# Optimization experiments

Measured on AMD Instinct MI355X. Metric: run time of the kernel, lower is better.

Reference implementation:

```python
import jax, jax.numpy as jnp
import numpy as np

D_MODEL = 192
D_INNER = 384          # expand(2) * d_model
HEADDIM = 12
NHEADS = 32            # d_inner // headdim
DSTATE = 16
NGROUPS = 1
CONV_DIM = D_INNER + 2 * NGROUPS * DSTATE          # 416
D_IN_PROJ = 2 * D_INNER + 2 * NGROUPS * DSTATE + NHEADS  # 832
LN_EPS = 1e-5


def silu(x):
    return x * jax.nn.sigmoid(x)


def depthwise_conv2d(x_nchw, w, b):
    # groups == channels depthwise conv, kernel 3, padding 1 (SAME)
    out = jax.lax.conv_general_dilated(
        x_nchw, w, window_strides=(1, 1), padding='SAME',
        feature_group_count=CONV_DIM,
        dimension_numbers=('NCHW', 'OIHW', 'NCHW'))
    return out + b[None, :, None, None]


def setup_inputs() -> dict:
    key = jax.random.key(0)
    ks = jax.random.split(key, 10)
    Bn, H, W = 4, 128, 128
    u = jax.random.normal(ks[0], (Bn, H, W, D_MODEL), jnp.float32)
    t = jax.random.normal(ks[1], (Bn, H, W, D_MODEL), jnp.float32)
    s_in = 1.0 / np.sqrt(D_MODEL)
    W_in = jax.random.normal(ks[2], (D_IN_PROJ, D_MODEL), jnp.float32) * s_in
    W_t_in = jax.random.normal(ks[3], (D_IN_PROJ, D_MODEL), jnp.float32) * s_in
    conv_w = jax.random.normal(ks[4], (CONV_DIM, 1, 3, 3), jnp.float32) * (1.0 / 3.0)
    conv_b = jnp.zeros((CONV_DIM,), jnp.float32)
    # dt_bias = inverse-softplus of dt sampled log-uniform in [dt_min, dt_max]
    dt0 = jnp.exp(jax.random.uniform(ks[5], (NHEADS,)) * (np.log(0.1) - np.log(0.001)) + np.log(0.001))
    dt_bias = dt0 + jnp.log(-jnp.expm1(-dt0))
    A_log = jnp.log(jax.random.uniform(ks[6], (NHEADS,), minval=1.0, maxval=16.0))
    D = jnp.ones((NHEADS,), jnp.float32)
    ln_gamma = jnp.ones((D_INNER,), jnp.float32)
    ln_beta = jnp.zeros((D_INNER,), jnp.float32)
    W_out = jax.random.normal(ks[7], (D_MODEL, D_INNER), jnp.float32) * (1.0 / np.sqrt(D_INNER))
    return dict(u=u, t=t, W_in=W_in, W_t_in=W_t_in, conv_w=conv_w, conv_b=conv_b,
                dt_bias=dt_bias, A_log=A_log, D=D, ln_gamma=ln_gamma, ln_beta=ln_beta,
                W_out=W_out)


def reference(u, t, W_in, W_t_in, conv_w, conv_b, dt_bias, A_log, D,
              ln_gamma, ln_beta, W_out):
    B0, H, W_, C0 = u.shape
    L = H * W_
    uu = u.reshape(B0, L, C0)
    tt = t.reshape(B0, L, C0)

    # in_proj on main branch: split into z, xBC, dt
    zxbcdt = uu @ W_in.T                                    # (B, L, 832)
    z = zxbcdt[..., :D_INNER]                               # (B, L, 384)
    xBC = zxbcdt[..., D_INNER:D_INNER + CONV_DIM]           # (B, L, 416)
    dt = zxbcdt[..., D_INNER + CONV_DIM:]                   # (B, L, 32)
    dt = jax.nn.softplus(dt + dt_bias)

    # t branch: only x1B1C1 part is ultimately used (C := C1)
    x1B1C1 = (tt @ W_t_in.T)[..., D_INNER:D_INNER + CONV_DIM]

    # depthwise 3x3 conv + silu on both branches
    xBC = xBC.reshape(B0, H, W_, CONV_DIM).transpose(0, 3, 1, 2)
    xBC = silu(depthwise_conv2d(xBC, conv_w, conv_b))
    xBC = xBC.transpose(0, 2, 3, 1).reshape(B0, L, CONV_DIM)

    x1B1C1 = x1B1C1.reshape(B0, H, W_, CONV_DIM).transpose(0, 3, 1, 2)
    x1B1C1 = silu(depthwise_conv2d(x1B1C1, conv_w, conv_b))
    x1B1C1 = x1B1C1.transpose(0, 2, 3, 1).reshape(B0, L, CONV_DIM)

    x = xBC[..., :D_INNER]                                  # V features (B, L, 384)
    Bk = xBC[..., D_INNER:D_INNER + NGROUPS * DSTATE]       # K (B, L, 16)
    Cq = x1B1C1[..., D_INNER + NGROUPS * DSTATE:]           # Q from t-branch (B, L, 16)

    A = -jnp.exp(A_log)                                     # (nheads,), negative

    # non-causal linear attention duality (ngroups == 1)
    V = x.reshape(B0, L, NHEADS, HEADDIM).transpose(0, 2, 1, 3)   # (B, h, L, d)
    dtT = dt.transpose(0, 2, 1)                                   # (B, h, L)
    dA = -(dtT[..., None] * A[None, :, None, None])               # ssd_positve_dA: positive
    V_scaled = V * dA
    KV = jnp.einsum('bln,bhld->bhnd', Bk, V_scaled)               # (B, h, 16, 12)
    y = jnp.einsum('bln,bhnd->bhld', Cq, KV) + V * D[None, :, None, None]
    y = y.transpose(0, 2, 1, 3).reshape(B0, L, D_INNER)

    # LayerNorm over d_inner
    mu = jnp.mean(y, axis=-1, keepdims=True)
    var = jnp.mean((y - mu) ** 2, axis=-1, keepdims=True)
    y = (y - mu) * jax.lax.rsqrt(var + LN_EPS) * ln_gamma + ln_beta

    y = y * z
    out = y @ W_out.T
    return out.reshape(B0, H, W_, C0)
```

## Files before the change

kernel.cpp:

```cpp
#include <hip/hip_runtime.h>
#include <hip/hip_bf16.h>
#include <math.h>


#define BN 4
#define HH 128
#define WWID 128
#define LTOK (HH*WWID)
#define NTOK (BN*LTOK)
#define DMODEL 192
#define DINNER 384
#define NH 32
#define HD 12
#define DST 16
#define CONVD 416
#define KVCHUNKS 64
#define PM 256
#define PBN 64
#define BSTR 200

typedef __hip_bfloat16 bf16;
typedef unsigned int uint32;
typedef unsigned short ushort16;
typedef __attribute__((ext_vector_type(8))) short bf16x8;
typedef __attribute__((ext_vector_type(4))) float f32x4;
typedef __attribute__((ext_vector_type(16))) float f32x16;

__device__ __forceinline__ float bflo(uint32 v){ return __uint_as_float((v & 0xffffu) << 16); }
__device__ __forceinline__ float bfhi(uint32 v){ return __uint_as_float(v & 0xffff0000u); }
__device__ __forceinline__ ushort16 f2bf(float f){
    __hip_bfloat16 h = __float2bfloat16(f);
    return *reinterpret_cast<const ushort16*>(&h);
}
__device__ __forceinline__ float softplusf(float x){
    return (x > 20.f) ? x : log1pf(expf(x));
}
__device__ __forceinline__ float siluf(float x){
    return x / (1.f + expf(-x));
}

union BFPK { short s[8]; bf16x8 v; };

__global__ __launch_bounds__(256) void k_prep(
    const float* __restrict__ Win, const float* __restrict__ Wout,
    const float* __restrict__ cw,
    bf16* __restrict__ Winbf, bf16* __restrict__ Woutbf, float* __restrict__ wtr)
{
    const int i = blockIdx.x*256 + threadIdx.x;
    if (i < 832*DMODEL)   Winbf[i]  = __float2bfloat16(Win[i]);
    if (i < DMODEL*DINNER) Woutbf[i] = __float2bfloat16(Wout[i]);
    if (i < CONVD*9) { const int c = i/9, k = i - c*9; wtr[k*420 + c] = cw[i]; }
}

__global__ __launch_bounds__(512) void k_proj_mfma(
    const float* __restrict__ u, const bf16* __restrict__ Wbf,
    const float* __restrict__ dt_b, const float* __restrict__ A_log,
    bf16* __restrict__ z_bf, bf16* __restrict__ xbc_pre, float* __restrict__ dA)
{
    __shared__ __align__(16) short S[2][PBN*BSTR];

    const int tid = threadIdx.x;
    const int m0 = blockIdx.x * PM;
    const int wid = tid >> 6, lane = tid & 63;
    const int fr = lane & 31;
    const int hi = lane >> 5;

    bf16x8 a[12];
    {
        const float* arow = u + (size_t)(m0 + wid*32 + fr)*DMODEL;
        #pragma unroll
        for (int ks=0;ks<12;++ks) {
            const float4 a0 = *(const float4*)(arow + ks*16 + hi*8);
            const float4 a1 = *(const float4*)(arow + ks*16 + hi*8 + 4);
            BFPK pk;
            pk.s[0]=(short)f2bf(a0.x); pk.s[1]=(short)f2bf(a0.y);
            pk.s[2]=(short)f2bf(a0.z); pk.s[3]=(short)f2bf(a0.w);
            pk.s[4]=(short)f2bf(a1.x); pk.s[5]=(short)f2bf(a1.y);
            pk.s[6]=(short)f2bf(a1.z); pk.s[7]=(short)f2bf(a1.w);
            a[ks] = pk.v;
        }
    }

    const int srow = tid >> 3;
    const int sseg = tid & 7;
    uint4 r0, r1, r2;
    auto LOADB = [&](int nt) {
        const short* g = (const short*)Wbf + (size_t)(nt*PBN + srow)*DMODEL + sseg*24;
        r0 = *(const uint4*)g;
        r1 = *(const uint4*)(g + 8);
        r2 = *(const uint4*)(g + 16);
    };
    auto WRITEB = [&](int buf) {
        short* d = &S[buf][srow*BSTR + sseg*24];
        *(uint4*)d        = r0;
        *(uint4*)(d + 8)  = r1;
        *(uint4*)(d + 16) = r2;
    };

    LOADB(0); WRITEB(0);
    LOADB(1);
    __syncthreads();

    for (int nt = 0; nt < 13; ++nt) {
        const int cur = nt & 1;

        f32x16 acc0, acc1;
        #pragma unroll
        for (int i=0;i<16;++i) { acc0[i]=0.f; acc1[i]=0.f; }

        const short* Sb = &S[cur][0];
        #pragma unroll
        for (int ks=0;ks<12;++ks) {
            const bf16x8 b0 = *(const bf16x8*)&Sb[(fr     )*BSTR + ks*16 + hi*8];
            const bf16x8 b1 = *(const bf16x8*)&Sb[(32 + fr)*BSTR + ks*16 + hi*8];
            acc0 = __builtin_amdgcn_mfma_f32_32x32x16_bf16(a[ks], b0, acc0, 0, 0, 0);
            acc1 = __builtin_amdgcn_mfma_f32_32x32x16_bf16(a[ks], b1, acc1, 0, 0, 0);
        }

        #pragma unroll
        for (int ni=0;ni<2;++ni) {
            const f32x16& ac = ni ? acc1 : acc0;
            const int n0 = nt*64 + ni*32;
            const int n  = n0 + fr;
            if (n0 < DINNER) {
                #pragma unroll
                for (int r=0;r<16;++r) {
                    const int tok = m0 + wid*32 + (r&3) + 8*(r>>2) + 4*hi;
                    z_bf[(size_t)tok*DINNER + n] = __float2bfloat16(ac[r]);
                }
            } else if (n0 < 800) {
                #pragma unroll
                for (int r=0;r<16;++r) {
                    const int tok = m0 + wid*32 + (r&3) + 8*(r>>2) + 4*hi;
                    xbc_pre[(size_t)tok*CONVD + (n - DINNER)] = __float2bfloat16(ac[r]);
                }
            } else {
                const float db = dt_b[fr];
                const float al = expf(A_log[fr]);
                #pragma unroll
                for (int r=0;r<16;++r) {
                    const int tok = m0 + wid*32 + (r&3) + 8*(r>>2) + 4*hi;
                    const float dt = softplusf(ac[r] + db);
                    dA[(size_t)tok*NH + fr] = dt * al;
                }
            }
        }

        if (nt < 12) {
            WRITEB(cur ^ 1);
            if (nt < 11) LOADB(nt + 2);
        }
        __syncthreads();
    }
}

__global__ __launch_bounds__(256) void k_tproj(
    const float* __restrict__ t, const float* __restrict__ Wtin, float* __restrict__ cq_pre)
{
    __shared__ float ts[16][196];
    __shared__ float ws[16][196];
    const int tid = threadIdx.x;
    const int tok0 = blockIdx.x * 16;
    #pragma unroll
    for (int i = 0; i < 3; ++i) {
        const int flat = tid + 256*i;
        const int row = flat / 48, c = (flat % 48)*4;
        *(float4*)&ts[row][c] = *(const float4*)(t    + (size_t)(tok0+row)*DMODEL + c);
        *(float4*)&ws[row][c] = *(const float4*)(Wtin + (size_t)(784+row)*DMODEL + c);
    }
    __syncthreads();
    const int tt = tid >> 4, n = tid & 15;
    float s0=0.f,s1=0.f,s2=0.f,s3=0.f;
    #pragma unroll 4
    for (int k = 0; k < DMODEL; k += 4) {
        s0 = fmaf(ts[tt][k+0], ws[n][k+0], s0);
        s1 = fmaf(ts[tt][k+1], ws[n][k+1], s1);
        s2 = fmaf(ts[tt][k+2], ws[n][k+2], s2);
        s3 = fmaf(ts[tt][k+3], ws[n][k+3], s3);
    }
    cq_pre[(size_t)(tok0+tt)*DST + n] = (s0+s1)+(s2+s3);
}

__global__ __launch_bounds__(416) void k_conv416(
    const bf16* __restrict__ in, const float* __restrict__ wtr, const float* __restrict__ cb,
    bf16* __restrict__ out)
{
    __shared__ float ws[9*420];
    __shared__ float bs[416];
    const int tid = threadIdx.x;
    for (int i = tid; i < 9*420; i += 416) ws[i] = wtr[i];
    if (tid < 416) bs[tid] = cb[tid];
    __syncthreads();

    const int pl  = tid / 52;
    const int grp = tid - pl*52;
    const int c0  = grp*8;
    const int pix = blockIdx.x*8 + pl;
    const int hw  = pix & (LTOK-1);
    const int h = hw >> 7, w = hw & 127;
    const int bb = pix >> 14;

    float acc[8];
    {
        const float4 b0 = *(const float4*)&bs[c0];
        const float4 b1 = *(const float4*)&bs[c0+4];
        acc[0]=b0.x; acc[1]=b0.y; acc[2]=b0.z; acc[3]=b0.w;
        acc[4]=b1.x; acc[5]=b1.y; acc[6]=b1.z; acc[7]=b1.w;
    }

    #pragma unroll
    for (int dh=-1; dh<=1; ++dh) {
        const int hh = h + dh;
        if ((unsigned)hh >= (unsigned)HH) continue;
        #pragma unroll
        for (int dw=-1; dw<=1; ++dw) {
            const int w2 = w + dw;
            if ((unsigned)w2 >= (unsigned)WWID) continue;
            const int wi = (dh+1)*3 + (dw+1);
            const size_t off = ((size_t)((bb<<14) + (hh<<7) + w2))*CONVD + c0;
            const uint4 v = *(const uint4*)((const ushort16*)in + off);
            const float4 w0 = *(const float4*)&ws[wi*420 + c0];
            const float4 w1 = *(const float4*)&ws[wi*420 + c0 + 4];
            acc[0] = fmaf(bflo(v.x), w0.x, acc[0]);
            acc[1] = fmaf(bfhi(v.x), w0.y, acc[1]);
            acc[2] = fmaf(bflo(v.y), w0.z, acc[2]);
            acc[3] = fmaf(bfhi(v.y), w0.w, acc[3]);
            acc[4] = fmaf(bflo(v.z), w1.x, acc[4]);
            acc[5] = fmaf(bfhi(v.z), w1.y, acc[5]);
            acc[6] = fmaf(bflo(v.w), w1.z, acc[6]);
            acc[7] = fmaf(bfhi(v.w), w1.w, acc[7]);
        }
    }

    uint4 o;
    o.x = ((uint32)f2bf(siluf(acc[1])) << 16) | (uint32)f2bf(siluf(acc[0]));
    o.y = ((uint32)f2bf(siluf(acc[3])) << 16) | (uint32)f2bf(siluf(acc[2]));
    o.z = ((uint32)f2bf(siluf(acc[5])) << 16) | (uint32)f2bf(siluf(acc[4]));
    o.w = ((uint32)f2bf(siluf(acc[7])) << 16) | (uint32)f2bf(siluf(acc[6]));
    *(uint4*)((ushort16*)out + (size_t)pix*CONVD + c0) = o;
}

__global__ __launch_bounds__(256) void k_conv16(
    const float* __restrict__ in, const float* __restrict__ cw, const float* __restrict__ cb,
    float* __restrict__ out)
{
    const int idx = blockIdx.x*256 + threadIdx.x;
    const int cc = idx & 15;
    const int pix = idx >> 4;
    const int hw = pix & (LTOK-1);
    const int h = hw >> 7, w = hw & 127;
    const int bb = pix >> 14;
    const int c = 400 + cc;

    float wg[9];
    #pragma unroll
    for (int k=0;k<9;++k) wg[k] = cw[c*9+k];
    float a = cb[c];
    #pragma unroll
    for (int dh=-1; dh<=1; ++dh) {
        const int hh = h + dh;
        if ((unsigned)hh >= (unsigned)HH) continue;
        #pragma unroll
        for (int dw=-1; dw<=1; ++dw) {
            const int w2 = w + dw;
            if ((unsigned)w2 >= (unsigned)WWID) continue;
            a = fmaf(in[((size_t)((bb<<14)+(hh<<7)+w2))*16 + cc], wg[(dh+1)*3 + (dw+1)], a);
        }
    }
    out[(size_t)pix*16 + cc] = siluf(a);
}

__global__ __launch_bounds__(512) void k_kv(
    const bf16* __restrict__ xbc_post, const float* __restrict__ dA,
    float* __restrict__ partial)
{
    __shared__ short vsb[16][408];
    __shared__ float das[16][32];
    const int tid = threadIdx.x;
    const int b = blockIdx.y;
    const int n = tid & 15;
    const int g = tid >> 4;

    float acc[12];
    #pragma unroll
    for (int j=0;j<12;++j) acc[j]=0.f;

    const int l0base = b*LTOK + blockIdx.x*256;

    for (int it = 0; it < 16; ++it) {
        const int l0 = l0base + it*16;
        for (int i = tid; i < 16*200; i += 512) {
            const int tok = i / 200;
            const int c2 = i - tok*200;
            const uint32 v = *(const uint32*)((const ushort16*)xbc_post
                                + (size_t)(l0+tok)*CONVD + c2*2);
            *(uint32*)&vsb[tok][c2*2] = v;
        }
        {
            const int tok = tid >> 5, h = tid & 31;
            das[tok][h] = dA[(size_t)(l0+tok)*NH + h];
        }
        __syncthreads();

        #pragma unroll
        for (int tok = 0; tok < 16; ++tok) {
            const uint32 bkraw = (uint32)(ushort16)vsb[tok][DINNER + n];
            const float s = __uint_as_float(bkraw << 16) * das[tok][g];
            const uint32* vp = (const uint32*)&vsb[tok][g*12];
            const uint32 w0 = vp[0], w1 = vp[1], w2 = vp[2];
            acc[0]  = fmaf(s, bflo(w0), acc[0]);
            acc[1]  = fmaf(s, bfhi(w0), acc[1]);
            acc[2]  = fmaf(s, bflo(w1), acc[2]);
            acc[3]  = fmaf(s, bfhi(w1), acc[3]);
            acc[4]  = fmaf(s, bflo(w2), acc[4]);
            acc[5]  = fmaf(s, bfhi(w2), acc[5]);
            const uint32* vq = (const uint32*)&vsb[tok][g*12 + 6];
            const uint32 w3 = vq[0], w4 = vq[1], w5 = vq[2];
            acc[6]  = fmaf(s, bflo(w3), acc[6]);
            acc[7]  = fmaf(s, bfhi(w3), acc[7]);
            acc[8]  = fmaf(s, bflo(w4), acc[8]);
            acc[9]  = fmaf(s, bfhi(w4), acc[9]);
            acc[10] = fmaf(s, bflo(w5), acc[10]);
            acc[11] = fmaf(s, bfhi(w5), acc[11]);
        }
        __syncthreads();
    }

    float* dst = partial + ((size_t)(b*KVCHUNKS + blockIdx.x))*6144 + (size_t)tid*12;
    #pragma unroll
    for (int j4=0;j4<3;++j4)
        *(float4*)(dst + j4*4) = make_float4(acc[j4*4], acc[j4*4+1], acc[j4*4+2], acc[j4*4+3]);
}

__global__ __launch_bounds__(256) void k_kvred(
    const float* __restrict__ partial, float* __restrict__ kv)
{
    const int idx = blockIdx.x*256 + threadIdx.x;
    const int b = idx / 6144;
    const int flat = idx - b*6144;
    const float* p = partial + (size_t)(b*KVCHUNKS)*6144 + flat;
    float s = 0.f;
    #pragma unroll 4
    for (int c = 0; c < KVCHUNKS; ++c) s += p[(size_t)c*6144];
    kv[idx] = s;
}

__global__ __launch_bounds__(256) void k_ynorm(
    const bf16* __restrict__ xbc_post, const float* __restrict__ cq_post,
    const bf16* __restrict__ z_bf, const float* __restrict__ kv,
    const float* __restrict__ Dv, const float* __restrict__ ln_g, const float* __restrict__ ln_b,
    bf16* __restrict__ yz)
{
    __shared__ float kvs[NH*DST*HD];
    __shared__ float ys[16][386];
    __shared__ float cqs[16][16];
    const int tid = threadIdx.x;
    const int token0 = blockIdx.x * 16;
    const int b = token0 >> 14;

    for (int i = tid; i < NH*DST*HD; i += 256) {
        const int n = i / DINNER;
        const int hd = i - n*DINNER;
        const int h = hd / HD;
        const int d = hd - h*HD;
        kvs[i] = kv[((size_t)(b*NH + h)*DST + n)*HD + d];
    }
    {
        const int tt = tid >> 4, n2 = tid & 15;
        cqs[tt][n2] = cq_post[(size_t)(token0+tt)*DST + n2];
    }
    __syncthreads();

    #pragma unroll
    for (int jj=0; jj<12; ++jj) {
        const int flat = jj*256 + tid;
        const int tt = flat / 192;
        const int p  = flat - tt*192;
        const int hd = p*2;
        const int h = hd / HD;
        const int l = token0 + tt;
        const uint32 v = *(const uint32*)((const ushort16*)xbc_post + (size_t)l*CONVD + hd);
        const float dv = Dv[h];
        float a0 = bflo(v) * dv;
        float a1 = bfhi(v) * dv;
        #pragma unroll
        for (int n=0;n<16;++n) {
            const float c = cqs[tt][n];
            const float2 kk = *(const float2*)&kvs[n*DINNER + hd];
            a0 = fmaf(c, kk.x, a0);
            a1 = fmaf(c, kk.y, a1);
        }
        *(float2*)&ys[tt][hd] = make_float2(a0, a1);
    }
    __syncthreads();

    const int wave = tid >> 6, lane = tid & 63;
    #pragma unroll
    for (int i=0;i<4;++i) {
        const int tt = wave*4 + i;
        const int l = token0 + tt;
        float v[6]; float s=0.f, s2=0.f;
        #pragma unroll
        for (int k=0;k<6;++k){ const float x = ys[tt][k*64+lane]; v[k]=x; s+=x; s2=fmaf(x,x,s2); }
        #pragma unroll
        for (int off=32; off>0; off>>=1){ s += __shfl_xor(s,off,64); s2 += __shfl_xor(s2,off,64); }
        const float mu = s*(1.f/384.f);
        const float var = s2*(1.f/384.f) - mu*mu;
        const float rs = rsqrtf(var + 1e-5f);
        #pragma unroll
        for (int k=0;k<6;++k){
            const int idx = k*64+lane;
            const float yn = (v[k]-mu)*rs*ln_g[idx] + ln_b[idx];
            const uint32 zb = (uint32)(*((const ushort16*)z_bf + (size_t)l*DINNER + idx));
            const float zv = __uint_as_float(zb << 16);
            yz[(size_t)l*DINNER + idx] = __float2bfloat16(yn*zv);
        }
    }
}

__global__ __launch_bounds__(256) void k_out_mfma(
    const bf16* __restrict__ yz, const bf16* __restrict__ Wbf, float* __restrict__ out)
{
    __shared__ __align__(16) short As[2][128*40];
    __shared__ __align__(16) short Bs[2][192*40];

    const int tid = threadIdx.x;
    const int m0 = blockIdx.x * 128;
    const int wid = tid >> 6, lane = tid & 63;
    const int wm = wid >> 1, wn = wid & 1;
    const int fr = lane & 15, fq = lane >> 4;

    const int arow = tid >> 1, ahalf = tid & 1;
    auto stageA = [&](int ks, int buf) {
        const short* g = (const short*)yz + (size_t)(m0 + arow)*DINNER + ks*32 + ahalf*16;
        const uint4 v0 = *(const uint4*)g;
        const uint4 v1 = *(const uint4*)(g + 8);
        short* d = &As[buf][arow*40 + ahalf*16];
        *(uint4*)d = v0;
        *(uint4*)(d + 8) = v1;
    };
    auto stageB = [&](int ks, int buf) {
        #pragma unroll
        for (int i = 0; i < 3; ++i) {
            const int flat = tid + 256*i;
            const int row = flat >> 2, q = flat & 3;
            const uint4 v = *(const uint4*)((const short*)Wbf + (size_t)row*DINNER + ks*32 + q*8);
            *(uint4*)&Bs[buf][row*40 + q*8] = v;
        }
    };

    f32x4 acc[4][6];
    #pragma unroll
    for (int mi=0;mi<4;++mi)
        #pragma unroll
        for (int ni=0;ni<6;++ni) acc[mi][ni] = (f32x4){0.f,0.f,0.f,0.f};

    stageA(0, 0); stageB(0, 0);
    __syncthreads();

    const int aoff = (wm*64 + fr)*40 + fq*8;
    const int boff = (wn*96 + fr)*40 + fq*8;

    #pragma unroll
    for (int ks = 0; ks < 12; ++ks) {
        const int cur = ks & 1;
        if (ks < 11) { stageA(ks+1, cur^1); stageB(ks+1, cur^1); }
        bf16x8 a[4], b[6];
        #pragma unroll
        for (int mi=0;mi<4;++mi) a[mi] = *(const bf16x8*)(&As[cur][aoff + mi*640]);
        #pragma unroll
        for (int ni=0;ni<6;++ni) b[ni] = *(const bf16x8*)(&Bs[cur][boff + ni*640]);
        #pragma unroll
        for (int mi=0;mi<4;++mi)
            #pragma unroll
            for (int ni=0;ni<6;++ni)
                acc[mi][ni] = __builtin_amdgcn_mfma_f32_16x16x32_bf16(a[mi], b[ni], acc[mi][ni], 0, 0, 0);
        __syncthreads();
    }

    #pragma unroll
    for (int mi=0;mi<4;++mi) {
        #pragma unroll
        for (int j=0;j<4;++j) {
            const int tok = m0 + wm*64 + mi*16 + fq*4 + j;
            #pragma unroll
            for (int ni=0;ni<6;++ni) {
                const int n = wn*96 + ni*16 + fr;
                out[(size_t)tok*DMODEL + n] = acc[mi][ni][j];
            }
        }
    }
}

extern "C" void kernel_launch(void* const* d_in, const int* in_sizes, int n_in,
                              void* d_out, int out_size, void* d_ws, size_t ws_size,
                              hipStream_t stream)
{
    const float* u      = (const float*)d_in[0];
    const float* t      = (const float*)d_in[1];
    const float* Win    = (const float*)d_in[2];
    const float* Wtin   = (const float*)d_in[3];
    const float* conv_w = (const float*)d_in[4];
    const float* conv_b = (const float*)d_in[5];
    const float* dt_b   = (const float*)d_in[6];
    const float* A_log  = (const float*)d_in[7];
    const float* Dv     = (const float*)d_in[8];
    const float* ln_g   = (const float*)d_in[9];
    const float* ln_bt  = (const float*)d_in[10];
    const float* W_out  = (const float*)d_in[11];
    float* out = (float*)d_out;

    char* p = (char*)d_ws;
    bf16* z_bf     = (bf16*)p;  p += (size_t)NTOK*DINNER*2;
    bf16* xbc_pre  = (bf16*)p;  p += (size_t)NTOK*CONVD*2;
    bf16* xbc_post = (bf16*)p;  p += (size_t)NTOK*CONVD*2;
    float* cq_pre  = (float*)p; p += (size_t)NTOK*DST*4;
    float* cq_post = (float*)p; p += (size_t)NTOK*DST*4;
    float* dA      = (float*)p; p += (size_t)NTOK*NH*4;
    bf16* yz       = (bf16*)p;  p += (size_t)NTOK*DINNER*2;
    float* kv      = (float*)p; p += (size_t)BN*NH*DST*HD*4;
    bf16* Win_bf   = (bf16*)p;  p += (size_t)832*DMODEL*2;
    bf16* Wout_bf  = (bf16*)p;  p += (size_t)DMODEL*DINNER*2;
    float* wtr     = (float*)p; p += (size_t)9*420*4;

    float* kv_part = (float*)xbc_pre;

    k_prep<<<624, 256, 0, stream>>>(Win, W_out, conv_w, Win_bf, Wout_bf, wtr);
    k_proj_mfma<<<NTOK/PM, 512, 0, stream>>>(u, Win_bf, dt_b, A_log, z_bf, xbc_pre, dA);
    k_tproj<<<NTOK/16, 256, 0, stream>>>(t, Wtin, cq_pre);
    k_conv416<<<NTOK/8, 416, 0, stream>>>(xbc_pre, wtr, conv_b, xbc_post);
    k_conv16<<<NTOK*16/256, 256, 0, stream>>>(cq_pre, conv_w, conv_b, cq_post);
    k_kv<<<dim3(KVCHUNKS, BN), 512, 0, stream>>>(xbc_post, dA, kv_part);
    k_kvred<<<BN*6144/256, 256, 0, stream>>>(kv_part, kv);
    k_ynorm<<<NTOK/16, 256, 0, stream>>>(xbc_post, cq_post, z_bf, kv,
                                         Dv, ln_g, ln_bt, yz);
    k_out_mfma<<<512, 256, 0, stream>>>(yz, Wout_bf, out);
}
```

Before: 313.4 us.

## Pre-swizzle W_in into MFMA fragment layout and load B directly from global

```diff
diff --git a/kernel.cpp b/kernel.cpp
--- a/kernel.cpp
+++ b/kernel.cpp
@@ -15,9 +15,6 @@
 #define DST 16
 #define CONVD 416
 #define KVCHUNKS 64
-#define PM 256
-#define PBN 64
-#define BSTR 200
 
 typedef __hip_bfloat16 bf16;
 typedef unsigned int uint32;
@@ -44,30 +41,35 @@
 __global__ __launch_bounds__(256) void k_prep(
     const float* __restrict__ Win, const float* __restrict__ Wout,
     const float* __restrict__ cw,
-    bf16* __restrict__ Winbf, bf16* __restrict__ Woutbf, float* __restrict__ wtr)
+    bf16* __restrict__ Wsh, bf16* __restrict__ Woutbf, float* __restrict__ wtr)
 {
     const int i = blockIdx.x*256 + threadIdx.x;
-    if (i < 832*DMODEL)   Winbf[i]  = __float2bfloat16(Win[i]);
+    if (i < 832*DMODEL) {
+        const int idx8 = i >> 3, ii = i & 7;
+        const int ct  = idx8 / 768;
+        const int rem = idx8 - ct*768;
+        const int ks  = rem >> 6, lane = rem & 63;
+        const int ch  = ct*32 + (lane & 31);
+        const int k   = ks*16 + (lane >> 5)*8 + ii;
+        Wsh[i] = __float2bfloat16(Win[(size_t)ch*DMODEL + k]);
+    }
     if (i < DMODEL*DINNER) Woutbf[i] = __float2bfloat16(Wout[i]);
     if (i < CONVD*9) { const int c = i/9, k = i - c*9; wtr[k*420 + c] = cw[i]; }
 }
 
-__global__ __launch_bounds__(512) void k_proj_mfma(
-    const float* __restrict__ u, const bf16* __restrict__ Wbf,
+__global__ __launch_bounds__(256) void k_proj_mfma(
+    const float* __restrict__ u, const bf16* __restrict__ Wsh,
     const float* __restrict__ dt_b, const float* __restrict__ A_log,
     bf16* __restrict__ z_bf, bf16* __restrict__ xbc_pre, float* __restrict__ dA)
 {
-    __shared__ __align__(16) short S[2][PBN*BSTR];
-
     const int tid = threadIdx.x;
-    const int m0 = blockIdx.x * PM;
     const int wid = tid >> 6, lane = tid & 63;
-    const int fr = lane & 31;
-    const int hi = lane >> 5;
+    const int fr = lane & 31, hi = lane >> 5;
+    const int tokbase = blockIdx.x*128 + wid*32;
 
     bf16x8 a[12];
     {
-        const float* arow = u + (size_t)(m0 + wid*32 + fr)*DMODEL;
+        const float* arow = u + (size_t)(tokbase + fr)*DMODEL;
         #pragma unroll
         for (int ks=0;ks<12;++ks) {
             const float4 a0 = *(const float4*)(arow + ks*16 + hi*8);
@@ -81,76 +83,65 @@
         }
     }
 
-    const int srow = tid >> 3;
-    const int sseg = tid & 7;
-    uint4 r0, r1, r2;
-    auto LOADB = [&](int nt) {
-        const short* g = (const short*)Wbf + (size_t)(nt*PBN + srow)*DMODEL + sseg*24;
-        r0 = *(const uint4*)g;
-        r1 = *(const uint4*)(g + 8);
-        r2 = *(const uint4*)(g + 16);
+    const float db = dt_b[fr];
+    const float al = expf(A_log[fr]);
+
+    const short* gB = (const short*)Wsh + (size_t)lane*8;
+
+    auto epilogue = [&](int ct, const f32x16& ac) {
+        const int n = ct*32 + fr;
+        if (ct < 12) {
+            #pragma unroll
+            for (int r=0;r<16;++r) {
+                const int tok = tokbase + (r&3) + 8*(r>>2) + 4*hi;
+                z_bf[(size_t)tok*DINNER + n] = __float2bfloat16(ac[r]);
+            }
+        } else if (ct < 25) {
+            #pragma unroll
+            for (int r=0;r<16;++r) {
+                const int tok = tokbase + (r&3) + 8*(r>>2) + 4*hi;
+                xbc_pre[(size_t)tok*CONVD + (n - DINNER)] = __float2bfloat16(ac[r]);
+            }
+        } else {
+            #pragma unroll
+            for (int r=0;r<16;++r) {
+                const int tok = tokbase + (r&3) + 8*(r>>2) + 4*hi;
+                dA[(size_t)tok*NH + fr] = softplusf(ac[r] + db)*al;
+            }
+        }
     };
-    auto WRITEB = [&](int buf) {
-        short* d = &S[buf][srow*BSTR + sseg*24];
-        *(uint4*)d        = r0;
-        *(uint4*)(d + 8)  = r1;
-        *(uint4*)(d + 16) = r2;
-    };
-
-    LOADB(0); WRITEB(0);
-    LOADB(1);
-    __syncthreads();
-
-    for (int nt = 0; nt < 13; ++nt) {
-        const int cur = nt & 1;
-
-        f32x16 acc0, acc1;
-        #pragma unroll
-        for (int i=0;i<16;++i) { acc0[i]=0.f; acc1[i]=0.f; }
-
-        const short* Sb = &S[cur][0];
-        #pragma unroll
-        for (int ks=0;ks<12;++ks) {
-            const bf16x8 b0 = *(const bf16x8*)&Sb[(fr     )*BSTR + ks*16 + hi*8];
-            const bf16x8 b1 = *(const bf16x8*)&Sb[(32 + fr)*BSTR + ks*16 + hi*8];
-            acc0 = __builtin_amdgcn_mfma_f32_32x32x16_bf16(a[ks], b0, acc0, 0, 0, 0);
-            acc1 = __builtin_amdgcn_mfma_f32_32x32x16_bf16(a[ks], b1, acc1, 0, 0, 0);
-        }
-
-        #pragma unroll
-        for (int ni=0;ni<2;++ni) {
-            const f32x16& ac = ni ? acc1 : acc0;
-            const int n0 = nt*64 + ni*32;
-            const int n  = n0 + fr;
-            if (n0 < DINNER) {
-                #pragma unroll
-                for (int r=0;r<16;++r) {
-                    const int tok = m0 + wid*32 + (r&3) + 8*(r>>2) + 4*hi;
-                    z_bf[(size_t)tok*DINNER + n] = __float2bfloat16(ac[r]);
-                }
-            } else if (n0 < 800) {
-                #pragma unroll
-                for (int r=0;r<16;++r) {
-                    const int tok = m0 + wid*32 + (r&3) + 8*(r>>2) + 4*hi;
-                    xbc_pre[(size_t)tok*CONVD + (n - DINNER)] = __float2bfloat16(ac[r]);
-                }
-            } else {
-                const float db = dt_b[fr];
-                const float al = expf(A_log[fr]);
-                #pragma unroll
-                for (int r=0;r<16;++r) {
-                    const int tok = m0 + wid*32 + (r&3) + 8*(r>>2) + 4*hi;
-                    const float dt = softplusf(ac[r] + db);
-                    dA[(size_t)tok*NH + fr] = dt * al;
-                }
-            }
-        }
-
-        if (nt < 12) {
-            WRITEB(cur ^ 1);
-            if (nt < 11) LOADB(nt + 2);
-        }
-        __syncthreads();
+
+    bf16x8 bA[12], bB[12];
+    #pragma unroll
+    for (int ks=0;ks<12;++ks)
+        bA[ks] = *(const bf16x8*)(gB + (size_t)ks*512);
+
+    for (int ct = 0; ct < 26; ct += 2) {
+        #pragma unroll
+        for (int ks=0;ks<12;++ks)
+            bB[ks] = *(const bf16x8*)(gB + (size_t)((ct+1)*12 + ks)*512);
+
+        f32x16 acc;
+        #pragma unroll
+        for (int i=0;i<16;++i) acc[i]=0.f;
+        #pragma unroll
+        for (int ks=0;ks<12;++ks)
+            acc = __builtin_amdgcn_mfma_f32_32x32x16_bf16(a[ks], bA[ks], acc, 0, 0, 0);
+        epilogue(ct, acc);
+
+        if (ct + 2 < 26) {
+            #pragma unroll
+            for (int ks=0;ks<12;++ks)
+                bA[ks] = *(const bf16x8*)(gB + (size_t)((ct+2)*12 + ks)*512);
+        }
+
+        f32x16 acc2;
+        #pragma unroll
+        for (int i=0;i<16;++i) acc2[i]=0.f;
+        #pragma unroll
+        for (int ks=0;ks<12;++ks)
+            acc2 = __builtin_amdgcn_mfma_f32_32x32x16_bf16(a[ks], bB[ks], acc2, 0, 0, 0);
+        epilogue(ct+1, acc2);
     }
 }
 
@@ -519,14 +510,14 @@
     float* dA      = (float*)p; p += (size_t)NTOK*NH*4;
     bf16* yz       = (bf16*)p;  p += (size_t)NTOK*DINNER*2;
     float* kv      = (float*)p; p += (size_t)BN*NH*DST*HD*4;
-    bf16* Win_bf   = (bf16*)p;  p += (size_t)832*DMODEL*2;
+    bf16* Win_sh   = (bf16*)p;  p += (size_t)832*DMODEL*2;
     bf16* Wout_bf  = (bf16*)p;  p += (size_t)DMODEL*DINNER*2;
     float* wtr     = (float*)p; p += (size_t)9*420*4;
 
     float* kv_part = (float*)xbc_pre;
 
-    k_prep<<<624, 256, 0, stream>>>(Win, W_out, conv_w, Win_bf, Wout_bf, wtr);
-    k_proj_mfma<<<NTOK/PM, 512, 0, stream>>>(u, Win_bf, dt_b, A_log, z_bf, xbc_pre, dA);
+    k_prep<<<624, 256, 0, stream>>>(Win, W_out, conv_w, Win_sh, Wout_bf, wtr);
+    k_proj_mfma<<<NTOK/128, 256, 0, stream>>>(u, Win_sh, dt_b, A_log, z_bf, xbc_pre, dA);
     k_tproj<<<NTOK/16, 256, 0, stream>>>(t, Wtin, cq_pre);
     k_conv416<<<NTOK/8, 416, 0, stream>>>(xbc_pre, wtr, conv_b, xbc_post);
     k_conv16<<<NTOK*16/256, 256, 0, stream>>>(cq_pre, conv_w, conv_b, cq_post);
```

Result: slower. 326.9 us (+4.3%).
